# Kernel optimization log

Hardware: AMD Instinct MI355X
Metric: run time of the kernel (lower is better)

The kernel has to match this reference:

```python
import jax, jax.numpy as jnp
import numpy as np
from jax import lax

KS = 3
PAD = 1


def setup_inputs() -> dict:
    key = jax.random.key(0)
    k1, k2, k3 = jax.random.split(key, 3)
    b, c, h, w = 8, 64, 128, 128
    out_c = 64
    x = jax.random.normal(k1, (b, c, h, w), dtype=jnp.float32)
    # small offset weights keep predicted offsets in a sane range
    w_off = jax.random.normal(k2, (2 * KS * KS, c, KS, KS), dtype=jnp.float32) * 0.05
    b_off = jnp.zeros((2 * KS * KS,), dtype=jnp.float32)
    w_reg = jax.random.normal(k3, (out_c, c * KS * KS), dtype=jnp.float32) * 0.02
    b_reg = jnp.zeros((out_c,), dtype=jnp.float32)
    return {"x": x, "w_off": w_off, "b_off": b_off, "w_reg": w_reg, "b_reg": b_reg}


def _deform_forward(x, w_off, b_off, w_reg, b_reg):
    ks, pad = KS, PAD
    b, c, h, w = x.shape
    # offset conv: 3x3, stride 1, pad 1 -> [b, 2*ks*ks, h, w]
    offset = lax.conv_general_dilated(
        x, w_off, window_strides=(1, 1), padding=[(pad, pad), (pad, pad)],
        dimension_numbers=("NCHW", "OIHW", "NCHW"))
    offset = offset + b_off[None, :, None, None]

    # pad input (zeros), as in the torch module
    xp = jnp.pad(x, ((0, 0), (0, 0), (pad, pad), (pad, pad)))
    Hp, Wp = h + 2 * pad, w + 2 * pad

    dt = x.dtype
    # base grid p0: [...,0] = column (x), [...,1] = row (y)
    yy, xx = jnp.meshgrid(jnp.arange(h, dtype=dt), jnp.arange(w, dtype=dt), indexing="ij")
    # kernel offsets p_n: flattened k = i*ks + j -> (lin[j], lin[i])
    lin = jnp.linspace(-(ks - 1) // 2, (ks - 1) // 2, ks).astype(dt)
    pn_i, pn_j = jnp.meshgrid(lin, lin, indexing="ij")
    pn = jnp.stack([pn_j, pn_i], axis=-1).reshape(ks * ks, 2)  # [ks2, 2]

    # offsets: [b, ks2, 2, h, w] -> [b, ks2, h, w, 2]; [...,0]=x off, [...,1]=y off
    off = offset.reshape(b, ks * ks, 2, h, w).transpose(0, 1, 3, 4, 2)

    px = xx[None, None] + pn[None, :, 0, None, None] + off[..., 0]  # [b, ks2, h, w]
    py = yy[None, None] + pn[None, :, 1, None, None] + off[..., 1]

    # torch normalizes by UNPADDED (w-1, h-1) but samples the PADDED tensor with
    # align_corners=True; reproduce exactly: q = p/(dim-1) * (dim_pad-1)
    qx = px / (w - 1) * (Wp - 1)
    qy = py / (h - 1) * (Hp - 1)

    x0 = jnp.floor(qx)
    y0 = jnp.floor(qy)
    wx1 = qx - x0  # frac weights
    wy1 = qy - y0
    wx0 = 1.0 - wx1
    wy0 = 1.0 - wy1
    ix0 = x0.astype(jnp.int32)
    iy0 = y0.astype(jnp.int32)
    ix1 = ix0 + 1
    iy1 = iy0 + 1

    def corner(iy, ix):
        valid = ((iy >= 0) & (iy < Hp) & (ix >= 0) & (ix < Wp)).astype(dt)
        iyc = jnp.clip(iy, 0, Hp - 1)
        ixc = jnp.clip(ix, 0, Wp - 1)
        # gather per batch: img [c,Hp,Wp], idx [ks2,h,w] -> [c,ks2,h,w]
        vals = jax.vmap(lambda img, a, bb: img[:, a, bb])(xp, iyc, ixc)
        return vals * valid[:, None]  # broadcast over channel dim

    v00 = corner(iy0, ix0)
    v01 = corner(iy0, ix1)
    v10 = corner(iy1, ix0)
    v11 = corner(iy1, ix1)

    wy0e = wy0[:, None]; wy1e = wy1[:, None]
    wx0e = wx0[:, None]; wx1e = wx1[:, None]
    sampled = (v00 * wy0e * wx0e + v01 * wy0e * wx1e +
               v10 * wy1e * wx0e + v11 * wy1e * wx1e)  # [b, c, ks2, h, w]

    # layout matches torch: [b, c*ks2, h, w] with (c, kk) order
    xs = sampled.reshape(b, c * ks * ks, h, w)
    out = jnp.einsum("bkhw,ok->bohw", xs, w_reg) + b_reg[None, :, None, None]
    return out


def reference(x, w_off, b_off, w_reg, b_reg):
    return _deform_forward(x, w_off, b_off, w_reg, b_reg)
```

## Files before the change

### kernel.cpp

```cpp
#include <hip/hip_runtime.h>
#include <math.h>

#define HH 128
#define WW 128
#define CC 64
#define BB 8
#define OC 64
#define OFFC 18
#define HW (HH*WW)
#define HP 136
#define WP 136
#define PHW (HP*WP)

typedef __attribute__((ext_vector_type(8))) _Float16 f16x8;
typedef __attribute__((ext_vector_type(4))) float f32x4;

#define P_OFF      0
#define P_SIZE     (BB*32*PHW)
#define OFFS_OFF   (P_OFF + P_SIZE)
#define OFFS_SIZE  (BB*OFFC*HW)
#define WAREG_OFF  (OFFS_OFF + OFFS_SIZE)
#define WAREG_SIZE 18432
#define WAOFF_OFF  (WAREG_OFF + WAREG_SIZE)

#define PAD_BLOCKS 4624
#define PREP_BLOCKS 144

__device__ __forceinline__ unsigned short f2h(float f) {
    _Float16 t = (_Float16)f;
    unsigned short s;
    __builtin_memcpy(&s, &t, 2);
    return s;
}
__device__ __forceinline__ f16x8 u4_to_h8(uint4 u) {
    union { uint4 u; f16x8 h; } c; c.u = u; return c.h;
}
__device__ __forceinline__ uint4 h8_to_u4(f16x8 h) {
    union { uint4 u; f16x8 h; } c; c.h = h; return c.u;
}
__device__ __forceinline__ f16x8 splat8(float f) {
    _Float16 t = (_Float16)f;
    return (f16x8){t, t, t, t, t, t, t, t};
}

__global__ __launch_bounds__(256) void prep_pad_kernel(
    const float* __restrict__ x, uint4* __restrict__ P,
    const float* __restrict__ w_reg, const float* __restrict__ w_off,
    unsigned short* __restrict__ wA_reg, unsigned short* __restrict__ wA_off)
{
    int bid = blockIdx.x;
    int tid = threadIdx.x;
    if (bid < PAD_BLOCKS) {
        int idx = bid * 256 + tid;
        int pos = idx % PHW;
        int ig  = idx / PHW;
        int r   = pos / WP;
        int col = pos % WP;
        union { uint4 u; f16x8 h; } cv;
        cv.u = make_uint4(0u, 0u, 0u, 0u);
        if (r >= 4 && r <= 131 && col >= 4 && col <= 131) {
            const float* src = x + (ig * 8) * HW + (r - 4) * WW + (col - 4);
            #pragma unroll
            for (int e = 0; e < 8; ++e)
                cv.h[e] = (_Float16)src[e * HW];
        }
        P[idx] = cv.u;
    } else {
        int i = (bid - PAD_BLOCKS) * 256 + tid;
        if (i < 18 * 64 * 32) {
            int j = i & 7, quad = (i >> 3) & 3, o = (i >> 5) & 63, ks = i >> 11;
            int kt = ks >> 1, kk = ks & 1;
            int c = kk * 32 + quad * 8 + j;
            wA_reg[i] = f2h(w_reg[o * 576 + c * 9 + kt]);
        }
        if (i < 18 * 32 * 32) {
            int j = i & 7, quad = (i >> 3) & 3, o = (i >> 5) & 31, ks = i >> 10;
            int kt = ks >> 1, kk = ks & 1;
            int c = kk * 32 + quad * 8 + j;
            float v = (o < OFFC) ? w_off[(o * CC + c) * 9 + kt] : 0.0f;
            wA_off[i] = f2h(v);
        }
    }
}

struct Gather8 {
    uint4 a00, a01, a10, a11;
    uint4 b00, b01, b10, b11;
    float wx1, wy1;
};

__device__ __forceinline__ Gather8 issue_tap(
    const uint4* __restrict__ xq0, const uint4* __restrict__ xq1,
    int wv, int hv, int dx, int dy, float offx, float offy)
{
    const float scale = 129.0f / 127.0f;
    float pxf = ((float)wv + (float)dx) + offx;
    float pyf = ((float)hv + (float)dy) + offy;
    float qx = fminf(fmaxf(pxf * scale, -100.0f), 300.0f);
    float qy = fminf(fmaxf(pyf * scale, -100.0f), 300.0f);
    float x0f = floorf(qx), y0f = floorf(qy);
    Gather8 g;
    g.wx1 = qx - x0f;
    g.wy1 = qy - y0f;
    int ix0 = (int)x0f, iy0 = (int)y0f;
    int c0 = min(max(ix0 + 3, 0), WP - 2);
    int r0 = min(max(iy0 + 3, 0), HP - 1);
    int r1 = min(max(iy0 + 4, 0), HP - 1);
    int pr0 = r0 * WP + c0, pr1 = r1 * WP + c0;
    g.a00 = xq0[pr0]; g.a01 = xq0[pr0 + 1];
    g.a10 = xq0[pr1]; g.a11 = xq0[pr1 + 1];
    g.b00 = xq1[pr0]; g.b01 = xq1[pr0 + 1];
    g.b10 = xq1[pr1]; g.b11 = xq1[pr1 + 1];
    return g;
}

__device__ __forceinline__ void blend_write(
    uint4* __restrict__ dst, int qp, int pxl, const Gather8& g)
{
    f16x8 wx1v = splat8(g.wx1), wx0v = splat8(1.0f - g.wx1);
    f16x8 wy1v = splat8(g.wy1), wy0v = splat8(1.0f - g.wy1);
    f16x8 r0a = u4_to_h8(g.a00) * wx0v + u4_to_h8(g.a01) * wx1v;
    f16x8 r1a = u4_to_h8(g.a10) * wx0v + u4_to_h8(g.a11) * wx1v;
    dst[(qp * 2 + 0) * 64 + pxl] = h8_to_u4(r0a * wy0v + r1a * wy1v);
    f16x8 r0b = u4_to_h8(g.b00) * wx0v + u4_to_h8(g.b01) * wx1v;
    f16x8 r1b = u4_to_h8(g.b10) * wx0v + u4_to_h8(g.b11) * wx1v;
    dst[(qp * 2 + 1) * 64 + pxl] = h8_to_u4(r0b * wy0v + r1b * wy1v);
}

__global__ __launch_bounds__(256, 4) void fused_deform_kernel(
    const uint4* __restrict__ P, const unsigned short* __restrict__ wA_off,
    const float* __restrict__ b_off, const unsigned short* __restrict__ wA_reg,
    const float* __restrict__ b_reg, float* __restrict__ out)
{
    __shared__ uint4 shbuf[3 * 8 * 66];
    __shared__ float offs_lds[OFFC * 64];
    int img  = blockIdx.x & 7;
    int rest = blockIdx.x >> 3;
    int half = rest & 1;
    int pblk = rest >> 1;
    int tid  = threadIdx.x;
    int pxl  = tid & 63;
    int qp   = tid >> 6;
    int lane = tid & 63;
    int wvid = tid >> 6;
    int wv = half * 64 + pxl;
    int hv = pblk;

    for (int i = tid; i < 3 * 8 * 66; i += 256) {
        int r   = i / 528;
        int rem = i - r * 528;
        int g   = rem / 66;
        int j   = rem - g * 66;
        shbuf[(r * 8 + g) * 66 + j] =
            P[(img * 8 + g) * PHW + (pblk + 3 + r) * WP + (half * 64 + 3 + j)];
    }
    __syncthreads();

    {
        int s2  = wvid & 1;
        int ph2 = wvid >> 1;
        const f16x8* wOv = (const f16x8*)wA_off;
        const f16x8* xsc = (const f16x8*)shbuf;
        f32x4 oacc[2];
        oacc[0] = (f32x4){0.f, 0.f, 0.f, 0.f};
        oacc[1] = (f32x4){0.f, 0.f, 0.f, 0.f};
        for (int tap = 0; tap < 9; ++tap) {
            int dy = tap / 3, dx = tap % 3;
            f16x8 a0 = wOv[((tap * 2 + 0) * 32 + s2 * 16 + (lane & 15)) * 4 + (lane >> 4)];
            f16x8 a1 = wOv[((tap * 2 + 1) * 32 + s2 * 16 + (lane & 15)) * 4 + (lane >> 4)];
            #pragma unroll
            for (int pt = 0; pt < 2; ++pt) {
                int sj = ph2 * 32 + pt * 16 + (lane & 15) + dx;
                f16x8 b0 = xsc[(dy * 8 + (lane >> 4)) * 66 + sj];
                oacc[pt] = __builtin_amdgcn_mfma_f32_16x16x32_f16(a0, b0, oacc[pt], 0, 0, 0);
                f16x8 b1 = xsc[(dy * 8 + 4 + (lane >> 4)) * 66 + sj];
                oacc[pt] = __builtin_amdgcn_mfma_f32_16x16x32_f16(a1, b1, oacc[pt], 0, 0, 0);
            }
        }
        #pragma unroll
        for (int r = 0; r < 4; ++r) {
            int o = s2 * 16 + (lane >> 4) * 4 + r;
            if (o < OFFC) {
                float bias = b_off[o];
                #pragma unroll
                for (int pt = 0; pt < 2; ++pt) {
                    int p = ph2 * 32 + pt * 16 + (lane & 15);
                    offs_lds[o * 64 + p] = oacc[pt][r] + bias;
                }
            }
        }
    }
    __syncthreads();

    const f16x8* wAv = (const f16x8*)wA_reg;
    const uint4* xq0 = P + (img * 8 + qp * 2 + 0) * PHW;
    const uint4* xq1 = P + (img * 8 + qp * 2 + 1) * PHW;
    int aidx = (wvid * 16 + (lane & 15)) * 4 + (lane >> 4);

    f32x4 acc[4];
    #pragma unroll
    for (int pt = 0; pt < 4; ++pt) acc[pt] = (f32x4){0.f, 0.f, 0.f, 0.f};

    float ox = offs_lds[0 * 64 + pxl], oy = offs_lds[1 * 64 + pxl];
    Gather8 cur = issue_tap(xq0, xq1, wv, hv, -1, -1, ox, oy);
    f16x8 a0c = wAv[0 * 256 + aidx];
    f16x8 a1c = wAv[1 * 256 + aidx];

    #pragma unroll
    for (int tap = 0; tap < 9; ++tap) {
        uint4* dst = shbuf + (tap & 1) * 512;
        blend_write(dst, qp, pxl, cur);

        Gather8 nxt;
        f16x8 a0n, a1n;
        if (tap < 8) {
            int dx1 = (tap + 1) % 3 - 1, dy1 = (tap + 1) / 3 - 1;
            float oxn = offs_lds[(2 * tap + 2) * 64 + pxl];
            float oyn = offs_lds[(2 * tap + 3) * 64 + pxl];
            nxt = issue_tap(xq0, xq1, wv, hv, dx1, dy1, oxn, oyn);
            a0n = wAv[((tap + 1) * 2 + 0) * 256 + aidx];
            a1n = wAv[((tap + 1) * 2 + 1) * 256 + aidx];
        }

        asm volatile("s_waitcnt lgkmcnt(0)" ::: "memory");
        __builtin_amdgcn_s_barrier();
        asm volatile("" ::: "memory");

        const f16x8* xsv = (const f16x8*)(shbuf + (tap & 1) * 512);
        #pragma unroll
        for (int pt = 0; pt < 4; ++pt) {
            int pxi = pt * 16 + (lane & 15);
            f16x8 b0 = xsv[(lane >> 4) * 64 + pxi];
            acc[pt] = __builtin_amdgcn_mfma_f32_16x16x32_f16(a0c, b0, acc[pt], 0, 0, 0);
            f16x8 b1 = xsv[(4 + (lane >> 4)) * 64 + pxi];
            acc[pt] = __builtin_amdgcn_mfma_f32_16x16x32_f16(a1c, b1, acc[pt], 0, 0, 0);
        }

        if (tap < 8) {
            cur = nxt; a0c = a0n; a1c = a1n;
        }
    }

    float* op = out + img * (OC * HW) + hv * WW + half * 64;
    #pragma unroll
    for (int r = 0; r < 4; ++r) {
        int o = wvid * 16 + (lane >> 4) * 4 + r;
        float bias = b_reg[o];
        #pragma unroll
        for (int pt = 0; pt < 4; ++pt)
            op[o * HW + pt * 16 + (lane & 15)] = acc[pt][r] + bias;
    }
}

extern "C" void kernel_launch(void* const* d_in, const int* in_sizes, int n_in,
                              void* d_out, int out_size, void* d_ws, size_t ws_size,
                              hipStream_t stream) {
    const float* x     = (const float*)d_in[0];
    const float* w_off = (const float*)d_in[1];
    const float* b_off = (const float*)d_in[2];
    const float* w_reg = (const float*)d_in[3];
    const float* b_reg = (const float*)d_in[4];
    float* out = (float*)d_out;
    float* ws  = (float*)d_ws;

    uint4* P      = (uint4*)(ws + P_OFF);
    unsigned short* wA_reg = (unsigned short*)(ws + WAREG_OFF);
    unsigned short* wA_off = (unsigned short*)(ws + WAOFF_OFF);

    prep_pad_kernel<<<PAD_BLOCKS + PREP_BLOCKS, 256, 0, stream>>>(
        x, P, w_reg, w_off, wA_reg, wA_off);
    fused_deform_kernel<<<2048, 256, 0, stream>>>(
        P, wA_off, b_off, wA_reg, b_reg, out);
}
```

Before: 145.2 us.

## Halve LDS footprint and raise occupancy target to eight blocks per CU

Cuts the offset-conv staging buffer to half the channel groups and loads the two halves in sequence, so shared memory per block shrinks roughly by half. The main loop becomes single-buffered, with a second barrier per tap. Weight fragments are no longer prefetched a tap ahead, which saves registers. Launch bounds go from 4 to 8 blocks per CU for more occupancy, at the cost of extra barriers, lost software prefetch and tighter register limits.

```diff
diff --git a/kernel.cpp b/kernel.cpp
--- a/kernel.cpp
+++ b/kernel.cpp
@@ -127,12 +127,12 @@
     dst[(qp * 2 + 1) * 64 + pxl] = h8_to_u4(r0b * wy0v + r1b * wy1v);
 }
 
-__global__ __launch_bounds__(256, 4) void fused_deform_kernel(
+__global__ __launch_bounds__(256, 8) void fused_deform_kernel(
     const uint4* __restrict__ P, const unsigned short* __restrict__ wA_off,
     const float* __restrict__ b_off, const unsigned short* __restrict__ wA_reg,
     const float* __restrict__ b_reg, float* __restrict__ out)
 {
-    __shared__ uint4 shbuf[3 * 8 * 66];
+    __shared__ uint4 stage[3 * 4 * 66];
     __shared__ float offs_lds[OFFC * 64];
     int img  = blockIdx.x & 7;
     int rest = blockIdx.x >> 3;
@@ -146,36 +146,35 @@
     int wv = half * 64 + pxl;
     int hv = pblk;
 
-    for (int i = tid; i < 3 * 8 * 66; i += 256) {
-        int r   = i / 528;
-        int rem = i - r * 528;
-        int g   = rem / 66;
-        int j   = rem - g * 66;
-        shbuf[(r * 8 + g) * 66 + j] =
-            P[(img * 8 + g) * PHW + (pblk + 3 + r) * WP + (half * 64 + 3 + j)];
-    }
-    __syncthreads();
-
     {
         int s2  = wvid & 1;
         int ph2 = wvid >> 1;
         const f16x8* wOv = (const f16x8*)wA_off;
-        const f16x8* xsc = (const f16x8*)shbuf;
         f32x4 oacc[2];
         oacc[0] = (f32x4){0.f, 0.f, 0.f, 0.f};
         oacc[1] = (f32x4){0.f, 0.f, 0.f, 0.f};
-        for (int tap = 0; tap < 9; ++tap) {
-            int dy = tap / 3, dx = tap % 3;
-            f16x8 a0 = wOv[((tap * 2 + 0) * 32 + s2 * 16 + (lane & 15)) * 4 + (lane >> 4)];
-            f16x8 a1 = wOv[((tap * 2 + 1) * 32 + s2 * 16 + (lane & 15)) * 4 + (lane >> 4)];
-            #pragma unroll
-            for (int pt = 0; pt < 2; ++pt) {
-                int sj = ph2 * 32 + pt * 16 + (lane & 15) + dx;
-                f16x8 b0 = xsc[(dy * 8 + (lane >> 4)) * 66 + sj];
-                oacc[pt] = __builtin_amdgcn_mfma_f32_16x16x32_f16(a0, b0, oacc[pt], 0, 0, 0);
-                f16x8 b1 = xsc[(dy * 8 + 4 + (lane >> 4)) * 66 + sj];
-                oacc[pt] = __builtin_amdgcn_mfma_f32_16x16x32_f16(a1, b1, oacc[pt], 0, 0, 0);
+        for (int kk = 0; kk < 2; ++kk) {
+            for (int i = tid; i < 3 * 4 * 66; i += 256) {
+                int r   = i / 264;
+                int rem = i - r * 264;
+                int gl  = rem / 66;
+                int j   = rem - gl * 66;
+                stage[(r * 4 + gl) * 66 + j] =
+                    P[(img * 8 + kk * 4 + gl) * PHW + (pblk + 3 + r) * WP + (half * 64 + 3 + j)];
             }
+            __syncthreads();
+            const f16x8* xsc = (const f16x8*)stage;
+            for (int tap = 0; tap < 9; ++tap) {
+                int dy = tap / 3, dx = tap % 3;
+                f16x8 a = wOv[((tap * 2 + kk) * 32 + s2 * 16 + (lane & 15)) * 4 + (lane >> 4)];
+                #pragma unroll
+                for (int pt = 0; pt < 2; ++pt) {
+                    int sj = ph2 * 32 + pt * 16 + (lane & 15) + dx;
+                    f16x8 b = xsc[(dy * 4 + (lane >> 4)) * 66 + sj];
+                    oacc[pt] = __builtin_amdgcn_mfma_f32_16x16x32_f16(a, b, oacc[pt], 0, 0, 0);
+                }
+            }
+            __syncthreads();
         }
         #pragma unroll
         for (int r = 0; r < 4; ++r) {
@@ -192,6 +191,7 @@
     }
     __syncthreads();
 
+    uint4* xs = stage;
     const f16x8* wAv = (const f16x8*)wA_reg;
     const uint4* xq0 = P + (img * 8 + qp * 2 + 0) * PHW;
     const uint4* xq1 = P + (img * 8 + qp * 2 + 1) * PHW;
@@ -203,30 +203,27 @@
 
     float ox = offs_lds[0 * 64 + pxl], oy = offs_lds[1 * 64 + pxl];
     Gather8 cur = issue_tap(xq0, xq1, wv, hv, -1, -1, ox, oy);
-    f16x8 a0c = wAv[0 * 256 + aidx];
-    f16x8 a1c = wAv[1 * 256 + aidx];
 
     #pragma unroll
     for (int tap = 0; tap < 9; ++tap) {
-        uint4* dst = shbuf + (tap & 1) * 512;
-        blend_write(dst, qp, pxl, cur);
+        blend_write(xs, qp, pxl, cur);
+
+        f16x8 a0c = wAv[(tap * 2 + 0) * 256 + aidx];
+        f16x8 a1c = wAv[(tap * 2 + 1) * 256 + aidx];
 
         Gather8 nxt;
-        f16x8 a0n, a1n;
         if (tap < 8) {
             int dx1 = (tap + 1) % 3 - 1, dy1 = (tap + 1) / 3 - 1;
             float oxn = offs_lds[(2 * tap + 2) * 64 + pxl];
             float oyn = offs_lds[(2 * tap + 3) * 64 + pxl];
             nxt = issue_tap(xq0, xq1, wv, hv, dx1, dy1, oxn, oyn);
-            a0n = wAv[((tap + 1) * 2 + 0) * 256 + aidx];
-            a1n = wAv[((tap + 1) * 2 + 1) * 256 + aidx];
         }
 
         asm volatile("s_waitcnt lgkmcnt(0)" ::: "memory");
         __builtin_amdgcn_s_barrier();
         asm volatile("" ::: "memory");
 
-        const f16x8* xsv = (const f16x8*)(shbuf + (tap & 1) * 512);
+        const f16x8* xsv = (const f16x8*)xs;
         #pragma unroll
         for (int pt = 0; pt < 4; ++pt) {
             int pxi = pt * 16 + (lane & 15);
@@ -236,9 +233,11 @@
             acc[pt] = __builtin_amdgcn_mfma_f32_16x16x32_f16(a1c, b1, acc[pt], 0, 0, 0);
         }
 
-        if (tap < 8) {
-            cur = nxt; a0c = a0n; a1c = a1n;
-        }
+        asm volatile("s_waitcnt lgkmcnt(0)" ::: "memory");
+        __builtin_amdgcn_s_barrier();
+        asm volatile("" ::: "memory");
+
+        if (tap < 8) cur = nxt;
     }
 
     float* op = out + img * (OC * HW) + hv * WW + half * 64;
```

Measured after the change: 230.1 us. +58.5%, slower.
